# Optimization experiments

Measured on AMD Instinct MI355X. Metric: run time of the kernel, lower is better.

## Reference

```python
import jax, jax.numpy as jnp
import numpy as np

N_NODES = 100000
N_EDGES = 1000000
D_FEAT = 64


def setup_inputs() -> dict:
    key = jax.random.key(0)
    k1, k2 = jax.random.split(key)
    x = jax.random.normal(k1, (N_NODES, D_FEAT), dtype=jnp.float32)
    es = jax.random.randint(k2, (2, N_EDGES), 0, N_NODES, dtype=jnp.int32)
    return {"x": x, "es": es}


def reference(x, es):
    # message (option='o2i'): col, row = es ; x_i = x[row], x_o = x[col]
    col, row = es[0], es[1]
    x_i = x[row]                              # [E, D]
    x_o = x[col]                              # [E, D]
    msg = jnp.concatenate([x_i, x_o], axis=-1)  # [E, 2D]
    n = x.shape[0]
    # aggregate: scatter-mean over idx=col
    summed = jax.ops.segment_sum(msg, col, num_segments=n)          # [N, 2D]
    ones = jnp.ones((es.shape[1],), dtype=x.dtype)
    count = jax.ops.segment_sum(ones, col, num_segments=n)          # [N]
    count = jnp.maximum(count, 1.0)[:, None]  # clamp(min=1), broadcast
    return summed / count
```

## Files before the change

### kernel.cpp

```cpp
#include <hip/hip_runtime.h>

#define D 64
#define SH 7
#define CPB 128
#define CH 4096


__global__ __launch_bounds__(256) void bucket_totals(
    const int* __restrict__ es, int* __restrict__ btotal, int NB, int E) {
  __shared__ int h[1024];
  for (int i = threadIdx.x; i < 1024; i += 256) h[i] = 0;
  __syncthreads();
  int e0 = blockIdx.x * CH + threadIdx.x;
#pragma unroll
  for (int j = 0; j < 16; j++) {
    int e = e0 + j * 256;
    if (e < E) atomicAdd(&h[es[e] >> SH], 1);
  }
  __syncthreads();
  for (int i = threadIdx.x; i < NB; i += 256) {
    int v = h[i];
    if (v) atomicAdd(&btotal[i], v);
  }
}

__global__ __launch_bounds__(256) void scan_buckets(
    const int* __restrict__ btotal, int* __restrict__ bbase,
    int* __restrict__ gcursor, int* __restrict__ offsets, int NB, int N, int E) {
  __shared__ int lds[256];
  int t = threadIdx.x;
  int v[4], s = 0;
#pragma unroll
  for (int i = 0; i < 4; i++) {
    int idx = t * 4 + i;
    v[i] = (idx < NB) ? btotal[idx] : 0;
    s += v[i];
  }
  lds[t] = s;
  __syncthreads();
  for (int off = 1; off < 256; off <<= 1) {
    int val = (t >= off) ? lds[t - off] : 0;
    __syncthreads();
    lds[t] += val;
    __syncthreads();
  }
  int run = (t == 0) ? 0 : lds[t - 1];
#pragma unroll
  for (int i = 0; i < 4; i++) {
    int idx = t * 4 + i;
    if (idx < NB) { bbase[idx] = run; gcursor[idx] = run; }
    run += v[i];
  }
  if (t == 0) { bbase[NB] = E; offsets[N] = E; }
}

__global__ __launch_bounds__(256) void bucket_scatter(
    const int* __restrict__ es, int* __restrict__ gcursor,
    int* __restrict__ packed, int NB, int E) {
  __shared__ int lhist[1024];
  __shared__ int delta[1024];
  __shared__ int sctmp[256];
  __shared__ int staged[CH];
  __shared__ int destg[CH];
  int t = threadIdx.x;
  for (int i = t; i < 1024; i += 256) lhist[i] = 0;
  __syncthreads();
  int base_e = blockIdx.x * CH;
#pragma unroll
  for (int j = 0; j < 16; j++) {
    int e = base_e + t + j * 256;
    if (e < E) atomicAdd(&lhist[es[e] >> SH], 1);
  }
  __syncthreads();
  int v[4], s = 0;
#pragma unroll
  for (int i = 0; i < 4; i++) { v[i] = lhist[t * 4 + i]; s += v[i]; }
  sctmp[t] = s;
  __syncthreads();
  for (int off = 1; off < 256; off <<= 1) {
    int val = (t >= off) ? sctmp[t - off] : 0;
    __syncthreads();
    sctmp[t] += val;
    __syncthreads();
  }
  int run = (t == 0) ? 0 : sctmp[t - 1];
  int lstart4[4];
#pragma unroll
  for (int i = 0; i < 4; i++) { lstart4[i] = run; run += v[i]; }
  __syncthreads();
#pragma unroll
  for (int i = 0; i < 4; i++) {
    int b = t * 4 + i;
    int gb = (b < NB && v[i] > 0) ? atomicAdd(&gcursor[b], v[i]) : 0;
    delta[b] = gb - lstart4[i];
    lhist[b] = lstart4[i];
  }
  __syncthreads();
#pragma unroll
  for (int j = 0; j < 16; j++) {
    int e = base_e + t + j * 256;
    if (e < E) {
      int c = es[e];
      int r = es[E + e];
      int b = c >> SH;
      int rank = atomicAdd(&lhist[b], 1);
      staged[rank] = (r << SH) | (c & (CPB - 1));
      destg[rank] = delta[b] + rank;
    }
  }
  __syncthreads();
  int nloc = min(CH, E - base_e);
  for (int i = t; i < nloc; i += 256) packed[destg[i]] = staged[i];
}

__global__ __launch_bounds__(256) void bucket_sort_cols(
    const int* __restrict__ packed, const int* __restrict__ bbase,
    int* __restrict__ offsets, int* __restrict__ sorted_rows, int N) {
  __shared__ int cnt[CPB];
  __shared__ int sc[CPB];
  __shared__ int cur[CPB];
  int b = blockIdx.x;
  int t = threadIdx.x;
  int s = bbase[b], e = bbase[b + 1];
  if (t < CPB) cnt[t] = 0;
  __syncthreads();
  for (int i = s + t; i < e; i += 256) atomicAdd(&cnt[packed[i] & (CPB - 1)], 1);
  __syncthreads();
  int v = (t < CPB) ? cnt[t] : 0;
  if (t < CPB) sc[t] = v;
  __syncthreads();
  for (int off = 1; off < CPB; off <<= 1) {
    int val = (t < CPB && t >= off) ? sc[t - off] : 0;
    __syncthreads();
    if (t < CPB) sc[t] += val;
    __syncthreads();
  }
  if (t < CPB) {
    int excl = sc[t] - v;
    cur[t] = excl;
    int gc = (b << SH) + t;
    if (gc < N) offsets[gc] = s + excl;
  }
  __syncthreads();
  for (int i = s + t; i < e; i += 256) {
    int p = packed[i];
    int c = p & (CPB - 1);
    int rank = atomicAdd(&cur[c], 1);
    sorted_rows[s + rank] = p >> SH;
  }
}

__global__ __launch_bounds__(256) void node_reduce(
    const float4* __restrict__ x4, const int* __restrict__ sorted_rows,
    const int* __restrict__ offsets, float* __restrict__ out, int N) {
  int gid = blockIdx.x * 256 + threadIdx.x;
  int node = gid >> 6;
  if (node >= N) return;
  int lane = threadIdx.x & 63;
  int eg = lane >> 4;
  int d16 = lane & 15;
  int start = offsets[node];
  int cnt = offsets[node + 1] - start;
  float4 a0 = make_float4(0.f, 0.f, 0.f, 0.f);
  float4 a1 = make_float4(0.f, 0.f, 0.f, 0.f);
  float4 a2 = make_float4(0.f, 0.f, 0.f, 0.f);
  float4 a3 = make_float4(0.f, 0.f, 0.f, 0.f);
  for (int base = 0; base < cnt; base += 16) {
    int k0 = base + eg;
    int k1 = base + 4 + eg;
    int k2 = base + 8 + eg;
    int k3 = base + 12 + eg;
    int r0 = (k0 < cnt) ? sorted_rows[start + k0] : -1;
    int r1 = (k1 < cnt) ? sorted_rows[start + k1] : -1;
    int r2 = (k2 < cnt) ? sorted_rows[start + k2] : -1;
    int r3 = (k3 < cnt) ? sorted_rows[start + k3] : -1;
    if (r0 >= 0) { float4 v = x4[(size_t)r0 * 16 + d16];
      a0.x += v.x; a0.y += v.y; a0.z += v.z; a0.w += v.w; }
    if (r1 >= 0) { float4 v = x4[(size_t)r1 * 16 + d16];
      a1.x += v.x; a1.y += v.y; a1.z += v.z; a1.w += v.w; }
    if (r2 >= 0) { float4 v = x4[(size_t)r2 * 16 + d16];
      a2.x += v.x; a2.y += v.y; a2.z += v.z; a2.w += v.w; }
    if (r3 >= 0) { float4 v = x4[(size_t)r3 * 16 + d16];
      a3.x += v.x; a3.y += v.y; a3.z += v.z; a3.w += v.w; }
  }
  a0.x += a1.x + a2.x + a3.x;
  a0.y += a1.y + a2.y + a3.y;
  a0.z += a1.z + a2.z + a3.z;
  a0.w += a1.w + a2.w + a3.w;
  a0.x += __shfl_xor(a0.x, 16); a0.y += __shfl_xor(a0.y, 16);
  a0.z += __shfl_xor(a0.z, 16); a0.w += __shfl_xor(a0.w, 16);
  a0.x += __shfl_xor(a0.x, 32); a0.y += __shfl_xor(a0.y, 32);
  a0.z += __shfl_xor(a0.z, 32); a0.w += __shfl_xor(a0.w, 32);
  float4* o4 = (float4*)(out + (size_t)node * 2 * D);
  if (eg == 0) {
    float inv = 1.0f / (float)(cnt > 0 ? cnt : 1);
    a0.x *= inv; a0.y *= inv; a0.z *= inv; a0.w *= inv;
    o4[d16] = a0;
  } else if (eg == 1) {
    float4 v = (cnt > 0) ? x4[(size_t)node * 16 + d16]
                         : make_float4(0.f, 0.f, 0.f, 0.f);
    o4[16 + d16] = v;
  }
}


__global__ __launch_bounds__(256) void edge_scatter_atomic(
    const int* __restrict__ es, const float* __restrict__ x,
    float* __restrict__ out, int* __restrict__ count, int E) {
  int gid = blockIdx.x * blockDim.x + threadIdx.x;
  int e = gid >> 6;
  int lane = gid & 63;
  if (e >= E) return;
  int c = es[e];
  int r = es[E + e];
  if (lane == 0) atomicAdd(&count[c], 1);
  float v = x[(size_t)r * D + lane];
  unsafeAtomicAdd(&out[(size_t)c * 2 * D + lane], v);
}

__global__ __launch_bounds__(256) void finalize_atomic(
    const float* __restrict__ x, float* __restrict__ out,
    const int* __restrict__ count, int N) {
  int gid = blockIdx.x * blockDim.x + threadIdx.x;
  int node = gid >> 5;
  int j4 = gid & 31;
  if (node >= N) return;
  int cnt = count[node];
  float4* out4 = (float4*)(out + (size_t)node * 2 * D);
  if (j4 < 16) {
    float4 s = out4[j4];
    float inv = 1.0f / (float)(cnt > 0 ? cnt : 1);
    s.x *= inv; s.y *= inv; s.z *= inv; s.w *= inv;
    out4[j4] = s;
  } else {
    float4 v;
    if (cnt > 0) {
      const float4* x4 = (const float4*)(x + (size_t)node * D);
      v = x4[j4 - 16];
    } else {
      v = make_float4(0.f, 0.f, 0.f, 0.f);
    }
    out4[j4] = v;
  }
}

extern "C" void kernel_launch(void* const* d_in, const int* in_sizes, int n_in,
                              void* d_out, int out_size, void* d_ws, size_t ws_size,
                              hipStream_t stream) {
  const float* x = (const float*)d_in[0];
  const int* es = (const int*)d_in[1];
  int N = in_sizes[0] / D;
  int E = in_sizes[1] / 2;
  float* out = (float*)d_out;

  int NB = (N + CPB - 1) >> SH;
  size_t need = ((size_t)3104 + (N + 1) + (size_t)2 * E) * sizeof(int);
  if (NB > 1024 || (1 << SH) * 131072 <= N || ws_size < need) {
    int* count = (int*)d_ws;
    hipMemsetAsync(count, 0, (size_t)N * sizeof(int), stream);
    hipMemsetAsync(out, 0, (size_t)N * 2 * D * sizeof(float), stream);
    long long t1 = (long long)E * 64;
    edge_scatter_atomic<<<(int)((t1 + 255) / 256), 256, 0, stream>>>(es, x, out, count, E);
    long long t2 = (long long)N * 32;
    finalize_atomic<<<(int)((t2 + 255) / 256), 256, 0, stream>>>(x, out, count, N);
    return;
  }

  int* ws = (int*)d_ws;
  int* btotal = ws;
  int* bbase = ws + 1024;
  int* gcursor = ws + 2080;
  int* offsets = ws + 3104;
  int* packed = offsets + N + 1;
  int* sorted_rows = packed + E;

  hipMemsetAsync(btotal, 0, 1024 * sizeof(int), stream);

  int B3 = (E + CH - 1) / CH;
  bucket_totals<<<B3, 256, 0, stream>>>(es, btotal, NB, E);
  scan_buckets<<<1, 256, 0, stream>>>(btotal, bbase, gcursor, offsets, NB, N, E);
  bucket_scatter<<<B3, 256, 0, stream>>>(es, gcursor, packed, NB, E);
  bucket_sort_cols<<<NB, 256, 0, stream>>>(packed, bbase, offsets, sorted_rows, N);

  long long rt = (long long)N * 64;
  node_reduce<<<(int)((rt + 255) / 256), 256, 0, stream>>>(
      (const float4*)x, sorted_rows, offsets, out, N);
}
```

Baseline: 175.9 us.

## Replace atomic bucket cursors with per-block count matrix scan, coarser buckets

The radix-style bucketing now writes per-block bucket histograms into a count matrix, scans it in one 1024-thread kernel, and uses those deterministic offsets in the scatter. This removes the memset and the global atomic cursor reservation. Buckets grow from 128 to 512 columns, so there are fewer buckets (196), fewer sort_cols blocks each doing more work, and fewer memory segments in the scatter. The risk is a serial per-thread loop in the single-block scan over about 48k entries, plus larger per-block sort work.

```diff
diff --git a/kernel.cpp b/kernel.cpp
--- a/kernel.cpp
+++ b/kernel.cpp
@@ -1,151 +1,150 @@
 #include <hip/hip_runtime.h>
 
 #define D 64
-#define SH 7
-#define CPB 128
+#define SH 9
+#define CPB 512
 #define CH 4096
-
-
-__global__ __launch_bounds__(256) void bucket_totals(
-    const int* __restrict__ es, int* __restrict__ btotal, int NB, int E) {
-  __shared__ int h[1024];
-  for (int i = threadIdx.x; i < 1024; i += 256) h[i] = 0;
-  __syncthreads();
-  int e0 = blockIdx.x * CH + threadIdx.x;
-#pragma unroll
-  for (int j = 0; j < 16; j++) {
-    int e = e0 + j * 256;
-    if (e < E) atomicAdd(&h[es[e] >> SH], 1);
-  }
-  __syncthreads();
-  for (int i = threadIdx.x; i < NB; i += 256) {
-    int v = h[i];
-    if (v) atomicAdd(&btotal[i], v);
-  }
-}
-
-__global__ __launch_bounds__(256) void scan_buckets(
-    const int* __restrict__ btotal, int* __restrict__ bbase,
-    int* __restrict__ gcursor, int* __restrict__ offsets, int NB, int N, int E) {
-  __shared__ int lds[256];
-  int t = threadIdx.x;
-  int v[4], s = 0;
-#pragma unroll
-  for (int i = 0; i < 4; i++) {
-    int idx = t * 4 + i;
-    v[i] = (idx < NB) ? btotal[idx] : 0;
-    s += v[i];
-  }
-  lds[t] = s;
-  __syncthreads();
-  for (int off = 1; off < 256; off <<= 1) {
-    int val = (t >= off) ? lds[t - off] : 0;
-    __syncthreads();
-    lds[t] += val;
-    __syncthreads();
-  }
-  int run = (t == 0) ? 0 : lds[t - 1];
-#pragma unroll
-  for (int i = 0; i < 4; i++) {
-    int idx = t * 4 + i;
-    if (idx < NB) { bbase[idx] = run; gcursor[idx] = run; }
-    run += v[i];
-  }
-  if (t == 0) { bbase[NB] = E; offsets[N] = E; }
-}
-
-__global__ __launch_bounds__(256) void bucket_scatter(
-    const int* __restrict__ es, int* __restrict__ gcursor,
-    int* __restrict__ packed, int NB, int E) {
-  __shared__ int lhist[1024];
-  __shared__ int delta[1024];
-  __shared__ int sctmp[256];
-  __shared__ int staged[CH];
-  __shared__ int destg[CH];
-  int t = threadIdx.x;
-  for (int i = t; i < 1024; i += 256) lhist[i] = 0;
+#define MAXNB 256
+
+
+__global__ __launch_bounds__(256) void count_kernel(
+    const int* __restrict__ es, int* __restrict__ cmat,
+    int NB, int NBLK, int E) {
+  __shared__ int hist[MAXNB];
+  int t = threadIdx.x;
+  hist[t] = 0;
   __syncthreads();
   int base_e = blockIdx.x * CH;
 #pragma unroll
   for (int j = 0; j < 16; j++) {
     int e = base_e + t + j * 256;
-    if (e < E) atomicAdd(&lhist[es[e] >> SH], 1);
-  }
-  __syncthreads();
-  int v[4], s = 0;
-#pragma unroll
-  for (int i = 0; i < 4; i++) { v[i] = lhist[t * 4 + i]; s += v[i]; }
-  sctmp[t] = s;
-  __syncthreads();
-  for (int off = 1; off < 256; off <<= 1) {
-    int val = (t >= off) ? sctmp[t - off] : 0;
-    __syncthreads();
-    sctmp[t] += val;
-    __syncthreads();
-  }
-  int run = (t == 0) ? 0 : sctmp[t - 1];
-  int lstart4[4];
-#pragma unroll
-  for (int i = 0; i < 4; i++) { lstart4[i] = run; run += v[i]; }
-  __syncthreads();
-#pragma unroll
-  for (int i = 0; i < 4; i++) {
-    int b = t * 4 + i;
-    int gb = (b < NB && v[i] > 0) ? atomicAdd(&gcursor[b], v[i]) : 0;
-    delta[b] = gb - lstart4[i];
-    lhist[b] = lstart4[i];
-  }
-  __syncthreads();
+    if (e < E) atomicAdd(&hist[es[e] >> SH], 1);
+  }
+  __syncthreads();
+  if (t < NB) cmat[t * NBLK + blockIdx.x] = hist[t];
+}
+
+__global__ __launch_bounds__(1024) void scan_kernel(
+    int* __restrict__ cmat, int* __restrict__ bbase,
+    int* __restrict__ offsets, int NB, int NBLK, int N, int E) {
+  __shared__ int lds[1024];
+  int t = threadIdx.x;
+  int M = NB * NBLK;
+  int per = (M + 1023) >> 10;
+  int lo = t * per, hi = min(M, lo + per);
+  int s = 0;
+  for (int i = lo; i < hi; i++) s += cmat[i];
+  lds[t] = s;
+  __syncthreads();
+  for (int off = 1; off < 1024; off <<= 1) {
+    int v = (t >= off) ? lds[t - off] : 0;
+    __syncthreads();
+    lds[t] += v;
+    __syncthreads();
+  }
+  int run = (t == 0) ? 0 : lds[t - 1];
+  for (int i = lo; i < hi; i++) {
+    int c = cmat[i];
+    cmat[i] = run;
+    if (i % NBLK == 0) bbase[i / NBLK] = run;
+    run += c;
+  }
+  if (t == 0) { bbase[NB] = E; offsets[N] = E; }
+}
+
+__global__ __launch_bounds__(256) void scatter_kernel(
+    const int* __restrict__ es, const int* __restrict__ cmat,
+    int* __restrict__ packed, int NB, int NBLK, int E) {
+  __shared__ int hist[MAXNB];
+  __shared__ int lstart[MAXNB];
+  __shared__ int gbase[MAXNB];
+  __shared__ int cursor[MAXNB];
+  __shared__ int sctmp[256];
+  __shared__ int staged[CH];
+  __shared__ int bidl[CH];
+  int t = threadIdx.x;
+  hist[t] = 0;
+  __syncthreads();
+  int base_e = blockIdx.x * CH;
+  int c[16], r[16];
 #pragma unroll
   for (int j = 0; j < 16; j++) {
     int e = base_e + t + j * 256;
     if (e < E) {
-      int c = es[e];
-      int r = es[E + e];
-      int b = c >> SH;
-      int rank = atomicAdd(&lhist[b], 1);
-      staged[rank] = (r << SH) | (c & (CPB - 1));
-      destg[rank] = delta[b] + rank;
+      c[j] = es[e];
+      r[j] = es[E + e];
+      atomicAdd(&hist[c[j] >> SH], 1);
+    } else {
+      c[j] = -1;
     }
   }
   __syncthreads();
+  int v = hist[t];
+  sctmp[t] = v;
+  __syncthreads();
+  for (int off = 1; off < 256; off <<= 1) {
+    int val = (t >= off) ? sctmp[t - off] : 0;
+    __syncthreads();
+    sctmp[t] += val;
+    __syncthreads();
+  }
+  int excl = sctmp[t] - v;
+  lstart[t] = excl;
+  cursor[t] = excl;
+  if (t < NB) gbase[t] = cmat[t * NBLK + blockIdx.x];
+  __syncthreads();
+#pragma unroll
+  for (int j = 0; j < 16; j++) {
+    if (c[j] >= 0) {
+      int b = c[j] >> SH;
+      int rank = atomicAdd(&cursor[b], 1);
+      staged[rank] = (r[j] << SH) | (c[j] & (CPB - 1));
+      bidl[rank] = b;
+    }
+  }
+  __syncthreads();
   int nloc = min(CH, E - base_e);
-  for (int i = t; i < nloc; i += 256) packed[destg[i]] = staged[i];
-}
-
-__global__ __launch_bounds__(256) void bucket_sort_cols(
+  for (int i = t; i < nloc; i += 256) {
+    int b = bidl[i];
+    packed[gbase[b] + (i - lstart[b])] = staged[i];
+  }
+}
+
+__global__ __launch_bounds__(256) void sort_cols(
     const int* __restrict__ packed, const int* __restrict__ bbase,
     int* __restrict__ offsets, int* __restrict__ sorted_rows, int N) {
   __shared__ int cnt[CPB];
-  __shared__ int sc[CPB];
+  __shared__ int sctmp[256];
   __shared__ int cur[CPB];
   int b = blockIdx.x;
   int t = threadIdx.x;
   int s = bbase[b], e = bbase[b + 1];
-  if (t < CPB) cnt[t] = 0;
+  cnt[t] = 0;
+  cnt[t + 256] = 0;
   __syncthreads();
   for (int i = s + t; i < e; i += 256) atomicAdd(&cnt[packed[i] & (CPB - 1)], 1);
   __syncthreads();
-  int v = (t < CPB) ? cnt[t] : 0;
-  if (t < CPB) sc[t] = v;
-  __syncthreads();
-  for (int off = 1; off < CPB; off <<= 1) {
-    int val = (t < CPB && t >= off) ? sc[t - off] : 0;
-    __syncthreads();
-    if (t < CPB) sc[t] += val;
-    __syncthreads();
-  }
-  if (t < CPB) {
-    int excl = sc[t] - v;
-    cur[t] = excl;
-    int gc = (b << SH) + t;
-    if (gc < N) offsets[gc] = s + excl;
-  }
+  int c0 = cnt[2 * t], c1 = cnt[2 * t + 1];
+  int pair = c0 + c1;
+  sctmp[t] = pair;
+  __syncthreads();
+  for (int off = 1; off < 256; off <<= 1) {
+    int val = (t >= off) ? sctmp[t - off] : 0;
+    __syncthreads();
+    sctmp[t] += val;
+    __syncthreads();
+  }
+  int excl = sctmp[t] - pair;
+  cur[2 * t] = excl;
+  cur[2 * t + 1] = excl + c0;
+  int gc0 = (b << SH) + 2 * t;
+  if (gc0 < N) offsets[gc0] = s + excl;
+  if (gc0 + 1 < N) offsets[gc0 + 1] = s + excl + c0;
   __syncthreads();
   for (int i = s + t; i < e; i += 256) {
     int p = packed[i];
-    int c = p & (CPB - 1);
-    int rank = atomicAdd(&cur[c], 1);
+    int cc = p & (CPB - 1);
+    int rank = atomicAdd(&cur[cc], 1);
     sorted_rows[s + rank] = p >> SH;
   }
 }
@@ -254,8 +253,10 @@
   float* out = (float*)d_out;
 
   int NB = (N + CPB - 1) >> SH;
-  size_t need = ((size_t)3104 + (N + 1) + (size_t)2 * E) * sizeof(int);
-  if (NB > 1024 || (1 << SH) * 131072 <= N || ws_size < need) {
+  int NBLK = (E + CH - 1) / CH;
+  size_t need = ((size_t)NB * NBLK + (NB + 1) + ((size_t)N + 1) +
+                 2 * (size_t)E) * sizeof(int);
+  if (NB > MAXNB || ws_size < need) {
     int* count = (int*)d_ws;
     hipMemsetAsync(count, 0, (size_t)N * sizeof(int), stream);
     hipMemsetAsync(out, 0, (size_t)N * 2 * D * sizeof(float), stream);
@@ -267,20 +268,16 @@
   }
 
   int* ws = (int*)d_ws;
-  int* btotal = ws;
-  int* bbase = ws + 1024;
-  int* gcursor = ws + 2080;
-  int* offsets = ws + 3104;
+  int* cmat = ws;
+  int* bbase = cmat + (size_t)NB * NBLK;
+  int* offsets = bbase + NB + 1;
   int* packed = offsets + N + 1;
   int* sorted_rows = packed + E;
 
-  hipMemsetAsync(btotal, 0, 1024 * sizeof(int), stream);
-
-  int B3 = (E + CH - 1) / CH;
-  bucket_totals<<<B3, 256, 0, stream>>>(es, btotal, NB, E);
-  scan_buckets<<<1, 256, 0, stream>>>(btotal, bbase, gcursor, offsets, NB, N, E);
-  bucket_scatter<<<B3, 256, 0, stream>>>(es, gcursor, packed, NB, E);
-  bucket_sort_cols<<<NB, 256, 0, stream>>>(packed, bbase, offsets, sorted_rows, N);
+  count_kernel<<<NBLK, 256, 0, stream>>>(es, cmat, NB, NBLK, E);
+  scan_kernel<<<1, 1024, 0, stream>>>(cmat, bbase, offsets, NB, NBLK, N, E);
+  scatter_kernel<<<NBLK, 256, 0, stream>>>(es, cmat, packed, NB, NBLK, E);
+  sort_cols<<<NB, 256, 0, stream>>>(packed, bbase, offsets, sorted_rows, N);
 
   long long rt = (long long)N * 64;
   node_reduce<<<(int)((rt + 255) / 256), 256, 0, stream>>>(
```

Measured after the change: 225.1 us. +27.9%, slower.
